# Optimization experiments

Measured on AMD Instinct MI355X. Metric: run time of the kernel, lower is better.

## Reference

```python
import jax, jax.numpy as jnp
from jax import lax
import numpy as np

B, T, K = 256, 512, 256
MAX_SEQ = 512  # max_sequence_length; output padded to MAX_SEQ + 2


def setup_inputs() -> dict:
    key = jax.random.key(0)
    k1, k2 = jax.random.split(key)
    emissions = jax.random.normal(k1, (B, T, K), dtype=jnp.float32)
    transitions = jax.random.normal(k2, (K, K), dtype=jnp.float32)
    mask = jnp.ones((B, T), dtype=jnp.int32)  # prefix mask; here full-length
    return {"emissions": emissions, "transitions": transitions, "mask": mask,
            "max_sequence_length": MAX_SEQ}


def _crf_decode(emissions, transitions, mask):
    # emissions: [B, T, K] float; transitions: [K, K]; mask: [B, T] int (prefix 1s)
    b, t, k = emissions.shape
    state0 = emissions[:, 0, :]                      # [B, K]
    em_rest = jnp.swapaxes(emissions[:, 1:, :], 0, 1)  # [T-1, B, K]
    mk_rest = jnp.swapaxes(mask[:, 1:], 0, 1)           # [T-1, B]

    def fwd(state, xs):
        em_t, mk_t = xs
        # scores[b, i, j] = state[b, i] + transitions[i, j]  (prev tag i -> cur tag j)
        scores = state[:, :, None] + transitions[None, :, :]   # [B, K, K]
        bp = jnp.argmax(scores, axis=1).astype(jnp.int32)       # [B, K] best prev tag
        new_state = jnp.max(scores, axis=1) + em_t              # [B, K]
        valid = (mk_t > 0)[:, None]
        # RNN-with-mask semantics: keep last valid state past sequence end
        return jnp.where(valid, new_state, state), bp

    last_state, bps = lax.scan(fwd, state0, (em_rest, mk_rest))  # bps: [T-1, B, K]
    last_tag = jnp.argmax(last_state, axis=-1).astype(jnp.int32)  # [B]

    def bwd(tag, xs):
        bp_t, mk_t = xs
        out = tag  # tag at this timestep
        prev = jnp.take_along_axis(bp_t, tag[:, None], axis=1)[:, 0]
        tag = jnp.where(mk_t > 0, prev, tag)  # only step back on valid positions
        return tag, out

    tag0, outs = lax.scan(bwd, last_tag, (bps, mk_rest), reverse=True)
    # outs[t] = tag at position t+1 (t = 0..T-2); tag0 = tag at position 0
    tags = jnp.concatenate([tag0[:, None], jnp.swapaxes(outs, 0, 1)], axis=1)  # [B, T]
    return tags


def reference(emissions, transitions, mask, max_sequence_length):
    tags = _crf_decode(emissions, transitions, mask)
    tags = tags * mask  # zero out padding positions
    pad = max_sequence_length + 2 - tags.shape[1]
    return jnp.pad(tags, ((0, 0), (0, pad)))
```

## Files before the change

kernel.cpp:

```cpp
#include <hip/hip_runtime.h>


#define TK 256
#define TT 512

typedef float v2f __attribute__((ext_vector_type(2)));

__device__ __forceinline__ float max3f(float a, float b, float c) {
  float d;
  asm("v_max3_f32 %0, %1, %2, %3" : "=v"(d) : "v"(a), "v"(b), "v"(c));
  return d;
}

__device__ __forceinline__ v2f pk_add(v2f a, v2f b) {
  v2f d;
  asm("v_pk_add_f32 %0, %1, %2" : "=v"(d) : "v"(a), "v"(b));
  return d;
}

__global__ void transpose_kernel(const float* __restrict__ trans,
                                 float* __restrict__ transT) {
  int j = blockIdx.x;
  int i = threadIdx.x;
  transT[(size_t)j * TK + i] = trans[(size_t)i * TK + j];
}

#define K16(X) X(0) X(1) X(2) X(3) X(4) X(5) X(6) X(7) \
               X(8) X(9) X(10) X(11) X(12) X(13) X(14) X(15)

__global__ __launch_bounds__(1024)
__attribute__((amdgpu_waves_per_eu(4, 4)))
void crf_fwd(const float* __restrict__ em,
             const float* __restrict__ transT,
             const int* __restrict__ mask,
             float* __restrict__ states) {
  const int b = blockIdx.x;
  const int tid = threadIdx.x;
  const int lane = tid & 63;
  const int w = tid >> 6;
  const int g = w >> 1;
  const int p = w & 1;
  const int j0 = 128 * p + 2 * lane;
  const int jm = 32 * g + (lane >> 1);

  __shared__ __align__(16) float st_w[16][32];
  __shared__ __align__(16) float part[2][8][TK];
  __shared__ int mk[TT];

  const float* ta = transT + (size_t)j0 * TK + 32 * g;
  const float* tb = ta + TK;
#define TRD(n) \
  const v2f TA##n = *reinterpret_cast<const v2f*>(ta + 2 * (n)); \
  const v2f TB##n = *reinterpret_cast<const v2f*>(tb + 2 * (n));
  K16(TRD)
#undef TRD

  if (tid < TT) mk[tid] = mask[(size_t)b * TT + tid];

  const size_t base = (size_t)b * TT * TK;
  float ns = em[base + jm];
  if ((lane & 1) == 0) {
    st_w[w][lane >> 1] = ns;
    if (p == 0) states[base + jm] = ns;
  }
  float em_n1 = em[base + TK + jm];
  float em_n2 = em[base + 2 * TK + jm];
  __syncthreads();

  const float* stw = st_w[w];

  for (int t = 1; t < TT; ++t) {
    const float em_cur = em_n1;
    em_n1 = em_n2;
    if (t + 2 < TT) em_n2 = em[base + (size_t)(t + 2) * TK + jm];

    v2f a0, b0;
    {
      const v2f SP = *reinterpret_cast<const v2f*>(stw);
      a0 = pk_add(TA0, SP);
      b0 = pk_add(TB0, SP);
    }
    float accx = fmaxf(a0.x, a0.y);
    float accy = fmaxf(b0.x, b0.y);
#define ROWK(n)                                                   \
    if ((n) > 0) {                                                \
      const v2f SP = *reinterpret_cast<const v2f*>(stw + 2 * (n));\
      const v2f aa = pk_add(TA##n, SP);                           \
      const v2f bb = pk_add(TB##n, SP);                           \
      accx = max3f(accx, aa.x, aa.y);                             \
      accy = max3f(accy, bb.x, bb.y);                             \
    }
    K16(ROWK)
#undef ROWK

    *reinterpret_cast<v2f*>(&part[t & 1][g][j0]) = (v2f){accx, accy};
    __syncthreads();

    const float* pb = &part[t & 1][4 * (lane & 1)][jm];
    const float v0 = pb[0];
    const float v1 = pb[TK];
    const float v2 = pb[2 * TK];
    const float v3 = pb[3 * TK];
    const float f = fmaxf(max3f(v0, v1, v2), v3);
    const float m = fmaxf(f, __shfl_xor(f, 1, 64));
    ns = (mk[t] > 0) ? (m + em_cur) : ns;
    if ((lane & 1) == 0) {
      st_w[w][lane >> 1] = ns;
      if (p == 0) states[base + (size_t)t * TK + jm] = ns;
    }
  }
}

__device__ __forceinline__ float wave_max(float m) {
#pragma unroll
  for (int d = 1; d < 64; d <<= 1) m = fmaxf(m, __shfl_xor(m, d, 64));
  return m;
}

__device__ __forceinline__ int first_eq_idx(float s0, float s1, float s2,
                                            float s3, float m) {
  unsigned long long b0 = __ballot(s0 == m);
  unsigned long long b1 = __ballot(s1 == m);
  unsigned long long b2 = __ballot(s2 == m);
  unsigned long long b3 = __ballot(s3 == m);
  int best = 0x7fffffff;
  if (b0) best = min(best, 4 * (__ffsll(b0) - 1) + 0);
  if (b1) best = min(best, 4 * (__ffsll(b1) - 1) + 1);
  if (b2) best = min(best, 4 * (__ffsll(b2) - 1) + 2);
  if (b3) best = min(best, 4 * (__ffsll(b3) - 1) + 3);
  return best;
}

__global__ __launch_bounds__(64, 1) void crf_bwd(const float* __restrict__ states,
                                                 const float* __restrict__ transT,
                                                 const int* __restrict__ mask,
                                                 int* __restrict__ out,
                                                 int out_stride) {
  const int b = blockIdx.x;
  const int lane = threadIdx.x;

  __shared__ int mk[TT];
  for (int q = lane; q < TT; q += 64) mk[q] = mask[(size_t)b * TT + q];
  __syncthreads();

  const size_t sbase = (size_t)b * TT * TK;
  int* outp = out + (size_t)b * out_stride;

  for (int q = TT + lane; q < out_stride; q += 64) outp[q] = 0;

  const float* srow = states + sbase;
  float4 r = *reinterpret_cast<const float4*>(srow + (size_t)(TT - 1) * TK + 4 * lane);
  float lm = fmaxf(fmaxf(r.x, r.y), fmaxf(r.z, r.w));
  lm = wave_max(lm);
  int tag = first_eq_idx(r.x, r.y, r.z, r.w, lm);

  auto LOADROW = [&](int rr) -> float4 {
    return *reinterpret_cast<const float4*>(srow + (size_t)rr * TK + 4 * lane);
  };
  float4 p0 = LOADROW(TT - 2), p1 = LOADROW(TT - 3), p2 = LOADROW(TT - 4),
         p3 = LOADROW(TT - 5);

  auto STEP = [&](float4 pr, int t) {
    int mkt = mk[t];
    if (lane == 0) outp[t] = (mkt > 0) ? tag : 0;
    const float4 tv =
        *reinterpret_cast<const float4*>(transT + (size_t)tag * TK + 4 * lane);
    float s0 = pr.x + tv.x;
    float s1 = pr.y + tv.y;
    float s2 = pr.z + tv.z;
    float s3 = pr.w + tv.w;
    float m = fmaxf(fmaxf(s0, s1), fmaxf(s2, s3));
    m = wave_max(m);
    int prev = first_eq_idx(s0, s1, s2, s3, m);
    tag = (mkt > 0) ? prev : tag;
  };

  int t = TT - 1;
  while (t >= 4) {
    STEP(p0, t);     if (t - 5 >= 0) p0 = LOADROW(t - 5);
    STEP(p1, t - 1); if (t - 6 >= 0) p1 = LOADROW(t - 6);
    STEP(p2, t - 2); if (t - 7 >= 0) p2 = LOADROW(t - 7);
    STEP(p3, t - 3); if (t - 8 >= 0) p3 = LOADROW(t - 8);
    t -= 4;
  }
  STEP(p0, 3);
  STEP(p1, 2);
  STEP(p2, 1);
  if (lane == 0) outp[0] = (mk[0] > 0) ? tag : 0;
}

extern "C" void kernel_launch(void* const* d_in, const int* in_sizes, int n_in,
                              void* d_out, int out_size, void* d_ws, size_t ws_size,
                              hipStream_t stream) {
  const float* em = (const float*)d_in[0];
  const float* trans = (const float*)d_in[1];
  const int* mask = (const int*)d_in[2];
  int* out = (int*)d_out;

  const int B = in_sizes[0] / (TT * TK);
  const int out_stride = out_size / B;

  float* states = (float*)d_ws;
  float* transT = states + (size_t)B * TT * TK;

  transpose_kernel<<<TK, TK, 0, stream>>>(trans, transT);
  crf_fwd<<<B, 1024, 0, stream>>>(em, transT, mask, states);
  crf_bwd<<<B, 64, 0, stream>>>(states, transT, mask, out, out_stride);
}
```

Measured before the change: 768.7 us.

## Restructure CRF forward reduction layout and use half-wave combine with raw barrier

Changes the shared partial-max buffer layout so each of 32 lanes reduces all 8 group partials directly, instead of every lane reading 4 and combining pairs through a cross-lane shuffle. State is read from LDS as eight 128-bit vector loads and added with plain scalar adds instead of inline packed-add asm. __syncthreads is replaced by an explicit lgkmcnt wait and s_barrier fenced with scheduling barriers. Only half of each wave now does the reduction, store and emission prefetch. This aims to shorten the serial per-timestep critical path, at the cost of more LDS reads per active lane.

```diff
diff --git a/kernel.cpp b/kernel.cpp
--- a/kernel.cpp
+++ b/kernel.cpp
@@ -5,16 +5,11 @@
 #define TT 512
 
 typedef float v2f __attribute__((ext_vector_type(2)));
+typedef float v4f __attribute__((ext_vector_type(4)));
 
 __device__ __forceinline__ float max3f(float a, float b, float c) {
   float d;
   asm("v_max3_f32 %0, %1, %2, %3" : "=v"(d) : "v"(a), "v"(b), "v"(c));
-  return d;
-}
-
-__device__ __forceinline__ v2f pk_add(v2f a, v2f b) {
-  v2f d;
-  asm("v_pk_add_f32 %0, %1, %2" : "=v"(d) : "v"(a), "v"(b));
   return d;
 }
 
@@ -41,72 +36,110 @@
   const int g = w >> 1;
   const int p = w & 1;
   const int j0 = 128 * p + 2 * lane;
-  const int jm = 32 * g + (lane >> 1);
 
   __shared__ __align__(16) float st_w[16][32];
-  __shared__ __align__(16) float part[2][8][TK];
+  __shared__ float part[2][8][2][2][64];
   __shared__ int mk[TT];
 
   const float* ta = transT + (size_t)j0 * TK + 32 * g;
-  const float* tb = ta + TK;
+  const float* tbq = ta + TK;
 #define TRD(n) \
   const v2f TA##n = *reinterpret_cast<const v2f*>(ta + 2 * (n)); \
-  const v2f TB##n = *reinterpret_cast<const v2f*>(tb + 2 * (n));
+  const v2f TB##n = *reinterpret_cast<const v2f*>(tbq + 2 * (n));
   K16(TRD)
 #undef TRD
 
   if (tid < TT) mk[tid] = mask[(size_t)b * TT + tid];
 
   const size_t base = (size_t)b * TT * TK;
-  float ns = em[base + jm];
-  if ((lane & 1) == 0) {
-    st_w[w][lane >> 1] = ns;
-    if (p == 0) states[base + jm] = ns;
+  const int pj = g >> 2;
+  const int sel = lane & 1;
+  const int col = 16 * (g & 3) + (lane >> 1);
+
+  float ns = 0.f, e1 = 0.f, e2 = 0.f;
+  if (lane < 32) {
+    ns = em[base + 32 * g + lane];
+    st_w[w][lane] = ns;
+    if (p == 0) states[base + 32 * g + lane] = ns;
+    e1 = em[base + TK + 32 * g + lane];
+    e2 = em[base + 2 * TK + 32 * g + lane];
   }
-  float em_n1 = em[base + TK + jm];
-  float em_n2 = em[base + 2 * TK + jm];
   __syncthreads();
 
-  const float* stw = st_w[w];
+  const float* emp = em + base + 3 * TK + 32 * g + lane;
+  float* stg = states + base + TK + 32 * g + lane;
+  const float* sw = st_w[w];
 
   for (int t = 1; t < TT; ++t) {
-    const float em_cur = em_n1;
-    em_n1 = em_n2;
-    if (t + 2 < TT) em_n2 = em[base + (size_t)(t + 2) * TK + jm];
-
-    v2f a0, b0;
+    const v4f S0 = reinterpret_cast<const v4f*>(sw)[0];
+    const v4f S1 = reinterpret_cast<const v4f*>(sw)[1];
+    const v4f S2 = reinterpret_cast<const v4f*>(sw)[2];
+    const v4f S3 = reinterpret_cast<const v4f*>(sw)[3];
+    const v4f S4 = reinterpret_cast<const v4f*>(sw)[4];
+    const v4f S5 = reinterpret_cast<const v4f*>(sw)[5];
+    const v4f S6 = reinterpret_cast<const v4f*>(sw)[6];
+    const v4f S7 = reinterpret_cast<const v4f*>(sw)[7];
+
+    float ax, ay;
     {
-      const v2f SP = *reinterpret_cast<const v2f*>(stw);
-      a0 = pk_add(TA0, SP);
-      b0 = pk_add(TB0, SP);
+      const float c0 = S0.x + TA0.x, c1 = S0.y + TA0.y;
+      ax = fmaxf(c0, c1);
+      const float d0 = S0.x + TB0.x, d1 = S0.y + TB0.y;
+      ay = fmaxf(d0, d1);
     }
-    float accx = fmaxf(a0.x, a0.y);
-    float accy = fmaxf(b0.x, b0.y);
-#define ROWK(n)                                                   \
-    if ((n) > 0) {                                                \
-      const v2f SP = *reinterpret_cast<const v2f*>(stw + 2 * (n));\
-      const v2f aa = pk_add(TA##n, SP);                           \
-      const v2f bb = pk_add(TB##n, SP);                           \
-      accx = max3f(accx, aa.x, aa.y);                             \
-      accy = max3f(accy, bb.x, bb.y);                             \
+#define STEP2(Sa, Sb, TAn, TBn)                                   \
+    {                                                             \
+      const float c0 = Sa + TAn.x, c1 = Sb + TAn.y;               \
+      ax = max3f(ax, c0, c1);                                     \
+      const float d0 = Sa + TBn.x, d1 = Sb + TBn.y;               \
+      ay = max3f(ay, d0, d1);                                     \
     }
-    K16(ROWK)
-#undef ROWK
-
-    *reinterpret_cast<v2f*>(&part[t & 1][g][j0]) = (v2f){accx, accy};
-    __syncthreads();
-
-    const float* pb = &part[t & 1][4 * (lane & 1)][jm];
-    const float v0 = pb[0];
-    const float v1 = pb[TK];
-    const float v2 = pb[2 * TK];
-    const float v3 = pb[3 * TK];
-    const float f = fmaxf(max3f(v0, v1, v2), v3);
-    const float m = fmaxf(f, __shfl_xor(f, 1, 64));
-    ns = (mk[t] > 0) ? (m + em_cur) : ns;
-    if ((lane & 1) == 0) {
-      st_w[w][lane >> 1] = ns;
-      if (p == 0) states[base + (size_t)t * TK + jm] = ns;
+    STEP2(S0.z, S0.w, TA1, TB1)
+    STEP2(S1.x, S1.y, TA2, TB2)
+    STEP2(S1.z, S1.w, TA3, TB3)
+    STEP2(S2.x, S2.y, TA4, TB4)
+    STEP2(S2.z, S2.w, TA5, TB5)
+    STEP2(S3.x, S3.y, TA6, TB6)
+    STEP2(S3.z, S3.w, TA7, TB7)
+    STEP2(S4.x, S4.y, TA8, TB8)
+    STEP2(S4.z, S4.w, TA9, TB9)
+    STEP2(S5.x, S5.y, TA10, TB10)
+    STEP2(S5.z, S5.w, TA11, TB11)
+    STEP2(S6.x, S6.y, TA12, TB12)
+    STEP2(S6.z, S6.w, TA13, TB13)
+    STEP2(S7.x, S7.y, TA14, TB14)
+    STEP2(S7.z, S7.w, TA15, TB15)
+#undef STEP2
+
+    float* pw = &part[t & 1][g][p][0][lane];
+    pw[0] = ax;
+    pw[64] = ay;
+
+    __builtin_amdgcn_sched_barrier(0);
+    asm volatile("s_waitcnt lgkmcnt(0)" ::: "memory");
+    __builtin_amdgcn_s_barrier();
+    __builtin_amdgcn_sched_barrier(0);
+
+    if (lane < 32) {
+      const float* pf = &part[t & 1][0][pj][sel][col];
+      const float f0 = pf[0];
+      const float f1 = pf[256];
+      const float f2 = pf[512];
+      const float f3 = pf[768];
+      const float f4 = pf[1024];
+      const float f5 = pf[1280];
+      const float f6 = pf[1536];
+      const float f7 = pf[1792];
+      float f = max3f(fmaxf(f0, f1), f2, f3);
+      f = max3f(f, f4, f5);
+      f = max3f(f, f6, f7);
+      ns = (mk[t] > 0) ? (f + e1) : ns;
+      st_w[w][lane] = ns;
+      if (p == 0) *stg = ns;
+      stg += TK;
+      e1 = e2;
+      if (t + 2 < TT) e2 = *emp;
+      emp += TK;
     }
   }
 }
```

New measurement: 794.4 us. 1.03x slower.
